# Optimization experiments

Measured on AMD Instinct MI355X. Metric: run time of the kernel, lower is better.

Reference implementation:

```python
import jax, jax.numpy as jnp
import numpy as np

IN_FEATURES = 4096
RANK = 64
NUM_EXPERTS = 8
ALPHA = 64.0
SPARSITY = 0.8
SCALING = ALPHA / RANK  # alpha / rank


def setup_inputs() -> dict:
    key = jax.random.key(0)
    k1, k2, k3, k4 = jax.random.split(key, 4)
    B, S = 4, 4096
    projected_input = jax.random.normal(k1, (B, S, RANK), dtype=jnp.float32)
    routing_weights = jax.random.uniform(k2, (B, S, NUM_EXPERTS), dtype=jnp.float32)
    # Stacked expert A matrices [K, in_features, rank] (kaiming-like init ~ normal here)
    A = jax.random.normal(k3, (NUM_EXPERTS, IN_FEATURES, RANK), dtype=jnp.float32) * 0.02
    sparse_mask = (jax.random.uniform(k4, (NUM_EXPERTS, IN_FEATURES, RANK)) >= SPARSITY).astype(jnp.float32)
    A = A * sparse_mask  # module masks A at init as well
    return {
        "projected_input": projected_input,
        "routing_weights": routing_weights,
        "A": A,
        "sparse_mask": sparse_mask,
    }


def reference(projected_input, routing_weights, A, sparse_mask):
    # A_sparse[k] = A[k] * mask[k]; per expert: scaling * (p @ A_sparse[k].T)
    # then weighted sum over experts with routing_weights[..., k].
    A_eff = (A * sparse_mask) * SCALING          # [k, d, r]
    # Weight the rank-projected input per expert, then contract:
    # wp[b,s,k,r] = routing_weights[b,s,k] * projected_input[b,s,r]
    wp = jnp.einsum("bsk,bsr->bskr", routing_weights, projected_input)
    out = jnp.einsum("bskr,kdr->bsd", wp, A_eff)  # [b, s, in_features]
    return out
```

## Files before the change

### kernel.cpp

```cpp
#include <hip/hip_runtime.h>

#define IN_FEATURES 4096
#define RANK 64
#define NUM_EXPERTS 8
#define KDIM 512
#define TOKENS 16384
#define SCALING 1.0f

#define BM 256
#define BN 256
#define BK 64
#define NKT (KDIM / BK)
#define NIT (NKT / 2)

typedef __bf16 bf16x8 __attribute__((ext_vector_type(8)));
typedef float f32x4 __attribute__((ext_vector_type(4)));

__device__ __forceinline__ unsigned short f2bf(float f) {
  union { float f; unsigned int u; } v; v.f = f;
  unsigned int u = v.u;
  u += 0x7fffu + ((u >> 16) & 1u);
  return (unsigned short)(u >> 16);
}

__device__ __forceinline__ void gload_lds16(const unsigned short* g, unsigned short* l) {
  __builtin_amdgcn_global_load_lds(
      (const __attribute__((address_space(1))) void*)g,
      (__attribute__((address_space(3))) void*)l,
      16, 0, 0);
}

#define QN4 ((long)TOKENS * KDIM / 4)
#define BN4 ((long)IN_FEATURES * KDIM / 4)
__global__ void __launch_bounds__(256) pack_both(
    const float* __restrict__ p, const float* __restrict__ w,
    const float* __restrict__ A, const float* __restrict__ mask,
    unsigned short* __restrict__ q, unsigned short* __restrict__ Bt) {
  long gid = (long)blockIdx.x * 256 + threadIdx.x;
  if (gid < QN4) {
    int idx = (int)gid;
    int t = idx >> 7;
    int k = (idx >> 4) & 7;
    int r0 = (idx & 15) * 4;
    float wk = w[t * NUM_EXPERTS + k];
    float4 pv = *(const float4*)&p[t * RANK + r0];
    ushort4 o;
    o.x = f2bf(wk * pv.x);
    o.y = f2bf(wk * pv.y);
    o.z = f2bf(wk * pv.z);
    o.w = f2bf(wk * pv.w);
    *(ushort4*)&q[(long)t * KDIM + k * RANK + r0] = o;
  } else {
    int idx = (int)(gid - QN4);
    int d = idx >> 7;
    int k = (idx >> 4) & 7;
    int r0 = (idx & 15) * 4;
    long src = ((long)k * IN_FEATURES + d) * RANK + r0;
    float4 a = *(const float4*)&A[src];
    float4 m = *(const float4*)&mask[src];
    ushort4 o;
    o.x = f2bf(a.x * m.x * SCALING);
    o.y = f2bf(a.y * m.y * SCALING);
    o.z = f2bf(a.z * m.z * SCALING);
    o.w = f2bf(a.w * m.w * SCALING);
    *(ushort4*)&Bt[(long)d * KDIM + k * RANK + r0] = o;
  }
}

__global__ void __launch_bounds__(512, 2) gemm_kernel(
    const unsigned short* __restrict__ q,
    const unsigned short* __restrict__ Bt,
    float* __restrict__ out) {
  __shared__ __align__(16) unsigned short sA[2][2][128 * BK];
  __shared__ __align__(16) unsigned short sB[2][2][128 * BK];

  const int tid = threadIdx.x;
  const int lane = tid & 63;
  const int wid = tid >> 6;
  const int u = lane & 15;
  const int quad = lane >> 4;
  const int hA = wid >> 2;
  const int hB = (wid & 3) >> 1;
  const int rB = (wid & 1) * 64;
  const int wn = (wid & 3) * 64;

  const int m0 = blockIdx.x * BM;
  const int n0 = blockIdx.y * BN;

  f32x4 acc[8][4];
#pragma unroll
  for (int i = 0; i < 8; ++i)
#pragma unroll
    for (int j = 0; j < 4; ++j)
      acc[i][j] = (f32x4){0.f, 0.f, 0.f, 0.f};

  const int c0 = tid, c1 = tid + 512;
  const int row0 = c0 >> 3, row1 = c1 >> 3;
  const int log0 = (c0 & 7) ^ (row0 & 7), log1 = (c1 & 7) ^ (row1 & 7);
  const unsigned short* gA0 = q + (m0 + row0) * KDIM + log0 * 8;
  const unsigned short* gA1 = q + (m0 + row1) * KDIM + log1 * 8;
  const unsigned short* gB0 = Bt + (n0 + row0) * KDIM + log0 * 8;
  const unsigned short* gB1 = Bt + (n0 + row1) * KDIM + log1 * 8;
  const int l0 = c0 * 8, l1 = c1 * 8;

  auto stageA = [&](int buf, int h, int kt) {
    int ko = (kt & (NKT - 1)) * BK + h * 128 * KDIM;
    gload_lds16(gA0 + ko, &sA[buf][h][l0]);
    gload_lds16(gA1 + ko, &sA[buf][h][l1]);
  };
  auto stageB = [&](int buf, int h, int kt) {
    int ko = (kt & (NKT - 1)) * BK + h * 128 * KDIM;
    gload_lds16(gB0 + ko, &sB[buf][h][l0]);
    gload_lds16(gB1 + ko, &sB[buf][h][l1]);
  };

  auto ldA = [&](int buf, int mq, bf16x8 (&a)[2][4]) {
    const unsigned short* base = sA[buf][hA];
#pragma unroll
    for (int ki = 0; ki < 2; ++ki)
#pragma unroll
      for (int f = 0; f < 4; ++f) {
        int r = mq * 64 + f * 16 + u;
        int phys = (ki * 4 + quad) ^ (r & 7);
        a[ki][f] = *(const bf16x8*)&base[r * BK + phys * 8];
      }
  };
  auto ldB = [&](int buf, int nq, bf16x8 (&b)[2][2]) {
    const unsigned short* base = sB[buf][hB];
#pragma unroll
    for (int ki = 0; ki < 2; ++ki)
#pragma unroll
      for (int g = 0; g < 2; ++g) {
        int r = rB + nq * 32 + g * 16 + u;
        int phys = (ki * 4 + quad) ^ (r & 7);
        b[ki][g] = *(const bf16x8*)&base[r * BK + phys * 8];
      }
  };
  auto mfmaQ = [&](int mq, int nq, bf16x8 (&a)[2][4], bf16x8 (&b)[2][2]) {
    __builtin_amdgcn_s_setprio(1);
#pragma unroll
    for (int ki = 0; ki < 2; ++ki)
#pragma unroll
      for (int f = 0; f < 4; ++f)
#pragma unroll
        for (int g = 0; g < 2; ++g)
          acc[mq * 4 + f][nq * 2 + g] = __builtin_amdgcn_mfma_f32_16x16x32_bf16(
              a[ki][f], b[ki][g], acc[mq * 4 + f][nq * 2 + g], 0, 0, 0);
    __builtin_amdgcn_s_setprio(0);
  };
  auto phase_bar = [&]() {
    __builtin_amdgcn_sched_barrier(0);
    __builtin_amdgcn_s_barrier();
  };

  bf16x8 Ar[2][4], B0r[2][2], B1r[2][2];

  stageB(0, 0, 0); stageB(0, 1, 0);
  stageA(0, 0, 0); stageA(0, 1, 0);
  stageB(1, 0, 1); stageB(1, 1, 1);
  asm volatile("s_waitcnt vmcnt(4)" ::: "memory");
  phase_bar();

  for (int i = 0; i < NIT; ++i) {
    const int k1 = 2 * i + 1, k2 = 2 * i + 2, k3 = 2 * i + 3;
    ldA(0, 0, Ar); ldB(0, 0, B0r);
    stageA(1, 0, k1);
    phase_bar();
    mfmaQ(0, 0, Ar, B0r);
    phase_bar();
    ldB(0, 1, B1r);
    stageA(1, 1, k1);
    phase_bar();
    mfmaQ(0, 1, Ar, B1r);
    phase_bar();
    ldA(0, 1, Ar);
    stageB(0, 0, k2);
    phase_bar();
    mfmaQ(1, 1, Ar, B1r);
    phase_bar();
    stageB(0, 1, k2);
    phase_bar();
    mfmaQ(1, 0, Ar, B0r);
    asm volatile("s_waitcnt vmcnt(4)" ::: "memory");
    phase_bar();
    ldA(1, 0, Ar); ldB(1, 0, B0r);
    stageA(0, 0, k2);
    phase_bar();
    mfmaQ(0, 0, Ar, B0r);
    phase_bar();
    ldB(1, 1, B1r);
    stageA(0, 1, k2);
    phase_bar();
    mfmaQ(0, 1, Ar, B1r);
    phase_bar();
    ldA(1, 1, Ar);
    stageB(1, 0, k3);
    phase_bar();
    mfmaQ(1, 1, Ar, B1r);
    phase_bar();
    stageB(1, 1, k3);
    phase_bar();
    mfmaQ(1, 0, Ar, B0r);
    asm volatile("s_waitcnt vmcnt(4)" ::: "memory");
    phase_bar();
  }

#pragma unroll
  for (int mf = 0; mf < 8; ++mf) {
    int row = m0 + hA * 128 + mf * 16 + quad * 4;
#pragma unroll
    for (int rr = 0; rr < 4; ++rr) {
      float* orow = out + (long)(row + rr) * IN_FEATURES + n0 + wn + u;
#pragma unroll
      for (int nf = 0; nf < 4; ++nf)
        orow[nf * 16] = acc[mf][nf][rr];
    }
  }
}

extern "C" void kernel_launch(void* const* d_in, const int* in_sizes, int n_in,
                              void* d_out, int out_size, void* d_ws, size_t ws_size,
                              hipStream_t stream) {
  const float* p    = (const float*)d_in[0];
  const float* w    = (const float*)d_in[1];
  const float* A    = (const float*)d_in[2];
  const float* mask = (const float*)d_in[3];
  float* out = (float*)d_out;

  unsigned short* q  = (unsigned short*)d_ws;
  unsigned short* Bt = q + (size_t)TOKENS * KDIM;

  int pack_blocks = (int)((QN4 + BN4) / 256);
  pack_both<<<pack_blocks, 256, 0, stream>>>(p, w, A, mask, q, Bt);

  dim3 grid(TOKENS / BM, IN_FEATURES / BN);
  gemm_kernel<<<grid, dim3(512), 0, stream>>>(q, Bt, out);
}
```

Measured before the change: 345.3 us.

## Replace phased 256x256 GEMM pipeline with simpler 256x128 double-buffered tiles

```diff
diff --git a/kernel.cpp b/kernel.cpp
--- a/kernel.cpp
+++ b/kernel.cpp
@@ -8,10 +8,9 @@
 #define SCALING 1.0f
 
 #define BM 256
-#define BN 256
-#define BK 64
+#define BN 128
+#define BK 32
 #define NKT (KDIM / BK)
-#define NIT (NKT / 2)
 
 typedef __bf16 bf16x8 __attribute__((ext_vector_type(8)));
 typedef float f32x4 __attribute__((ext_vector_type(4)));
@@ -67,153 +66,93 @@
   }
 }
 
-__global__ void __launch_bounds__(512, 2) gemm_kernel(
+__global__ void __launch_bounds__(512, 4) gemm_kernel(
     const unsigned short* __restrict__ q,
     const unsigned short* __restrict__ Bt,
     float* __restrict__ out) {
-  __shared__ __align__(16) unsigned short sA[2][2][128 * BK];
-  __shared__ __align__(16) unsigned short sB[2][2][128 * BK];
+  __shared__ __align__(16) unsigned short sA[2][BM * BK];
+  __shared__ __align__(16) unsigned short sB[2][BN * BK];
 
   const int tid = threadIdx.x;
   const int lane = tid & 63;
   const int wid = tid >> 6;
   const int u = lane & 15;
   const int quad = lane >> 4;
-  const int hA = wid >> 2;
-  const int hB = (wid & 3) >> 1;
-  const int rB = (wid & 1) * 64;
-  const int wn = (wid & 3) * 64;
+  const int wave_m = (wid >> 2) * 128;
+  const int wave_n = (wid & 3) * 32;
 
   const int m0 = blockIdx.x * BM;
   const int n0 = blockIdx.y * BN;
 
-  f32x4 acc[8][4];
+  f32x4 acc[8][2];
 #pragma unroll
   for (int i = 0; i < 8; ++i)
 #pragma unroll
-    for (int j = 0; j < 4; ++j)
+    for (int j = 0; j < 2; ++j)
       acc[i][j] = (f32x4){0.f, 0.f, 0.f, 0.f};
 
-  const int c0 = tid, c1 = tid + 512;
-  const int row0 = c0 >> 3, row1 = c1 >> 3;
-  const int log0 = (c0 & 7) ^ (row0 & 7), log1 = (c1 & 7) ^ (row1 & 7);
-  const unsigned short* gA0 = q + (m0 + row0) * KDIM + log0 * 8;
-  const unsigned short* gA1 = q + (m0 + row1) * KDIM + log1 * 8;
-  const unsigned short* gB0 = Bt + (n0 + row0) * KDIM + log0 * 8;
-  const unsigned short* gB1 = Bt + (n0 + row1) * KDIM + log1 * 8;
-  const int l0 = c0 * 8, l1 = c1 * 8;
+  const int cA0 = tid, cA1 = tid + 512, cB = tid;
+  const int rA0 = cA0 >> 2, rA1 = cA1 >> 2, rBr = cB >> 2;
+  const int lgA0 = (cA0 & 3) ^ ((rA0 >> 1) & 3);
+  const int lgA1 = (cA1 & 3) ^ ((rA1 >> 1) & 3);
+  const int lgB  = (cB  & 3) ^ ((rBr >> 1) & 3);
+  const unsigned short* gA0 = q  + (m0 + rA0) * KDIM + lgA0 * 8;
+  const unsigned short* gA1 = q  + (m0 + rA1) * KDIM + lgA1 * 8;
+  const unsigned short* gB  = Bt + (n0 + rBr) * KDIM + lgB  * 8;
+  const int lA0 = cA0 * 8, lA1 = cA1 * 8, lB = cB * 8;
 
-  auto stageA = [&](int buf, int h, int kt) {
-    int ko = (kt & (NKT - 1)) * BK + h * 128 * KDIM;
-    gload_lds16(gA0 + ko, &sA[buf][h][l0]);
-    gload_lds16(gA1 + ko, &sA[buf][h][l1]);
-  };
-  auto stageB = [&](int buf, int h, int kt) {
-    int ko = (kt & (NKT - 1)) * BK + h * 128 * KDIM;
-    gload_lds16(gB0 + ko, &sB[buf][h][l0]);
-    gload_lds16(gB1 + ko, &sB[buf][h][l1]);
+  auto stage = [&](int buf, int kt) {
+    int ko = (kt & (NKT - 1)) * BK;
+    gload_lds16(gA0 + ko, &sA[buf][lA0]);
+    gload_lds16(gA1 + ko, &sA[buf][lA1]);
+    gload_lds16(gB + ko, &sB[buf][lB]);
   };
 
-  auto ldA = [&](int buf, int mq, bf16x8 (&a)[2][4]) {
-    const unsigned short* base = sA[buf][hA];
+  stage(0, 0);
+  __syncthreads();
+
+  const int physv = quad ^ ((u >> 1) & 3);
+
+  for (int kt = 0; kt < NKT; ++kt) {
+    const int buf = kt & 1;
+    stage(buf ^ 1, kt + 1);
+
+    const unsigned short* bA = sA[buf];
+    const unsigned short* bB = sB[buf];
+
+    bf16x8 bfr[2];
 #pragma unroll
-    for (int ki = 0; ki < 2; ++ki)
+    for (int g = 0; g < 2; ++g) {
+      int r = wave_n + g * 16 + u;
+      bfr[g] = *(const bf16x8*)&bB[r * BK + physv * 8];
+    }
+#pragma unroll
+    for (int h = 0; h < 2; ++h) {
+      bf16x8 af[4];
 #pragma unroll
       for (int f = 0; f < 4; ++f) {
-        int r = mq * 64 + f * 16 + u;
-        int phys = (ki * 4 + quad) ^ (r & 7);
-        a[ki][f] = *(const bf16x8*)&base[r * BK + phys * 8];
+        int r = wave_m + (h * 4 + f) * 16 + u;
+        af[f] = *(const bf16x8*)&bA[r * BK + physv * 8];
       }
-  };
-  auto ldB = [&](int buf, int nq, bf16x8 (&b)[2][2]) {
-    const unsigned short* base = sB[buf][hB];
-#pragma unroll
-    for (int ki = 0; ki < 2; ++ki)
-#pragma unroll
-      for (int g = 0; g < 2; ++g) {
-        int r = rB + nq * 32 + g * 16 + u;
-        int phys = (ki * 4 + quad) ^ (r & 7);
-        b[ki][g] = *(const bf16x8*)&base[r * BK + phys * 8];
-      }
-  };
-  auto mfmaQ = [&](int mq, int nq, bf16x8 (&a)[2][4], bf16x8 (&b)[2][2]) {
-    __builtin_amdgcn_s_setprio(1);
-#pragma unroll
-    for (int ki = 0; ki < 2; ++ki)
 #pragma unroll
       for (int f = 0; f < 4; ++f)
 #pragma unroll
         for (int g = 0; g < 2; ++g)
-          acc[mq * 4 + f][nq * 2 + g] = __builtin_amdgcn_mfma_f32_16x16x32_bf16(
-              a[ki][f], b[ki][g], acc[mq * 4 + f][nq * 2 + g], 0, 0, 0);
-    __builtin_amdgcn_s_setprio(0);
-  };
-  auto phase_bar = [&]() {
-    __builtin_amdgcn_sched_barrier(0);
-    __builtin_amdgcn_s_barrier();
-  };
-
-  bf16x8 Ar[2][4], B0r[2][2], B1r[2][2];
-
-  stageB(0, 0, 0); stageB(0, 1, 0);
-  stageA(0, 0, 0); stageA(0, 1, 0);
-  stageB(1, 0, 1); stageB(1, 1, 1);
-  asm volatile("s_waitcnt vmcnt(4)" ::: "memory");
-  phase_bar();
-
-  for (int i = 0; i < NIT; ++i) {
-    const int k1 = 2 * i + 1, k2 = 2 * i + 2, k3 = 2 * i + 3;
-    ldA(0, 0, Ar); ldB(0, 0, B0r);
-    stageA(1, 0, k1);
-    phase_bar();
-    mfmaQ(0, 0, Ar, B0r);
-    phase_bar();
-    ldB(0, 1, B1r);
-    stageA(1, 1, k1);
-    phase_bar();
-    mfmaQ(0, 1, Ar, B1r);
-    phase_bar();
-    ldA(0, 1, Ar);
-    stageB(0, 0, k2);
-    phase_bar();
-    mfmaQ(1, 1, Ar, B1r);
-    phase_bar();
-    stageB(0, 1, k2);
-    phase_bar();
-    mfmaQ(1, 0, Ar, B0r);
-    asm volatile("s_waitcnt vmcnt(4)" ::: "memory");
-    phase_bar();
-    ldA(1, 0, Ar); ldB(1, 0, B0r);
-    stageA(0, 0, k2);
-    phase_bar();
-    mfmaQ(0, 0, Ar, B0r);
-    phase_bar();
-    ldB(1, 1, B1r);
-    stageA(0, 1, k2);
-    phase_bar();
-    mfmaQ(0, 1, Ar, B1r);
-    phase_bar();
-    ldA(1, 1, Ar);
-    stageB(1, 0, k3);
-    phase_bar();
-    mfmaQ(1, 1, Ar, B1r);
-    phase_bar();
-    stageB(1, 1, k3);
-    phase_bar();
-    mfmaQ(1, 0, Ar, B0r);
-    asm volatile("s_waitcnt vmcnt(4)" ::: "memory");
-    phase_bar();
+          acc[h * 4 + f][g] = __builtin_amdgcn_mfma_f32_16x16x32_bf16(
+              af[f], bfr[g], acc[h * 4 + f][g], 0, 0, 0);
+    }
+    __syncthreads();
   }
 
 #pragma unroll
-  for (int mf = 0; mf < 8; ++mf) {
-    int row = m0 + hA * 128 + mf * 16 + quad * 4;
+  for (int f = 0; f < 8; ++f) {
+    int row = m0 + wave_m + f * 16 + quad * 4;
 #pragma unroll
     for (int rr = 0; rr < 4; ++rr) {
-      float* orow = out + (long)(row + rr) * IN_FEATURES + n0 + wn + u;
+      float* orow = out + (long)(row + rr) * IN_FEATURES + n0 + wave_n + u;
 #pragma unroll
-      for (int nf = 0; nf < 4; ++nf)
-        orow[nf * 16] = acc[mf][nf][rr];
+      for (int g = 0; g < 2; ++g)
+        orow[g * 16] = acc[f][g][rr];
     }
   }
 }
```

New measurement: 342.6 us. About the same (-0.8%).
